# Performance work log

Measured on AMD Instinct MI355X. Metric: run time of the kernel, lower is better.

## Reference

```python
import jax, jax.numpy as jnp
import numpy as np

D, H, K, L, NB = 128, 8, 16, 16, 2
N, E, MN, ME = 100_000, 800_000, 1_000, 8_000
VOCAB, BT, VP = 50_000, 256, 15
_SQD, _SQK = float(np.sqrt(D)), float(np.sqrt(K))


def _segment_softmax(score, seg, num):
    m = jax.ops.segment_max(score, seg, num_segments=num)
    e = jnp.exp(score - m[seg])
    z = jax.ops.segment_sum(e, seg, num_segments=num)
    return e / (z[seg] + 1e-9)


def _meta_learner(feat, u, W2, W1):
    # latent-attention factorization: feat [n,D] -> 2d param [n,H,K], 1d param [n,H]
    w = jax.nn.softmax((feat @ u.T) / _SQD, axis=-1)  # [n,L]
    return jnp.einsum('nl,lhk->nhk', w, W2), w @ W1


def _conv(feat, src, dst, p2n, p1n, p2e, p1e, Wq, Wk, Wv, Wo):
    # HeteroAttnConv: multi-head attention message passing modulated by
    # per-node (p2n,p1n) and per-edge (p2e,p1e) meta parameters.
    n = feat.shape[0]
    q = (feat @ Wq).reshape(n, H, K) * p2n
    kf = (feat @ Wk).reshape(n, H, K)
    v = (feat @ Wv).reshape(n, H, K)
    ke = kf[src] * p2e                                   # [e,H,K]
    score = (q[dst] * ke).sum(-1) / _SQK + p1e + p1n[dst]  # [e,H]
    attn = _segment_softmax(score, dst, n)
    agg = jax.ops.segment_sum(attn[..., None] * v[src], dst, num_segments=n).reshape(n, D)
    return jax.nn.relu(agg @ Wo), ke.reshape(-1, D)


def _forward(emb, u, W2lat, W1lat, Wq_m, Wk_m, Wv_m, Wo_m, Wq, Wk, Wv, Wo,
             node_vals, meta_node_vals, src, dst, meta_src, meta_dst,
             meta_node_id, meta_edge_id, target_idx,
             static_vals, static_src, static_dst):
    # _init_meta_param: static param-name graph, copy_u/sum then meta_learner
    fs = emb[static_vals]
    agg = jax.ops.segment_sum(fs[static_src], static_dst, num_segments=VP)
    p2s, p1s = _meta_learner(agg, u, W2lat, W1lat)
    base_tw, base_n1, base_n2 = p1s[0], p1s[3], p2s[6]   # target_weight, node 1d, node 2d
    base_e1, base_e2 = p1s[9], p2s[12]                   # edge 1d, edge 2d

    meta_feat = emb[meta_node_vals]
    feat = emb[node_vals]
    # _asign_param_to_graph(meta_graph): broadcast base buffers only
    mp2n = jnp.broadcast_to(base_n2, (MN, H, K))
    mp1n = jnp.broadcast_to(base_n1, (MN, H))
    mp2e = jnp.broadcast_to(base_e2, (ME, H, K))
    mp1e = jnp.broadcast_to(base_e1, (ME, H))

    out = jnp.zeros((BT, 1), feat.dtype)
    for b in range(NB):
        pre_meta, pre = meta_feat, feat
        meta_feat, meta_edge_feat = _conv(meta_feat, meta_src, meta_dst,
                                          mp2n, mp1n, mp2e, mp1e,
                                          Wq_m[b], Wk_m[b], Wv_m[b], Wo_m[b])
        # _asign_param_to_graph(graph, meta_node_feat, meta_edge_feat):
        # base repeat + indexed add of meta_learner outputs
        p2mn, p1mn = _meta_learner(meta_feat, u, W2lat, W1lat)
        p2me, p1me = _meta_learner(meta_edge_feat, u, W2lat, W1lat)
        p2n = base_n2[None] + p2mn[meta_node_id]
        p1n = base_n1[None] + p1mn[meta_node_id]
        tw = base_tw[None] + p1mn[meta_node_id]
        p2e = base_e2[None] + p2me[meta_edge_id]
        p1e = base_e1[None] + p1me[meta_edge_id]
        feat, _ = _conv(feat, src, dst, p2n, p1n, p2e, p1e,
                        Wq[b], Wk[b], Wv[b], Wo[b])
        # block residual
        meta_feat = meta_feat + pre_meta
        feat = feat + pre
        # Target: per-target-node weighted readout with target_weight param
        logit = jnp.einsum('th,thk->t', tw[target_idx],
                           feat[target_idx].reshape(BT, H, K))
        out = out + logit[:, None]
    return out / NB


def setup_inputs() -> dict:
    key = jax.random.key(0)
    ks = jax.random.split(key, 24)
    s = 0.05
    inp = {}
    inp['emb'] = jax.random.normal(ks[0], (VOCAB, D), jnp.float32) * s
    inp['u'] = jax.random.normal(ks[1], (L, D), jnp.float32) * s
    inp['W2lat'] = jax.random.normal(ks[2], (L, H, K), jnp.float32) * s
    inp['W1lat'] = jax.random.normal(ks[3], (L, H), jnp.float32) * s
    for i, nm in enumerate(['Wq_m', 'Wk_m', 'Wv_m', 'Wo_m', 'Wq', 'Wk', 'Wv', 'Wo']):
        inp[nm] = jax.random.normal(ks[4 + i], (NB, D, D), jnp.float32) / np.sqrt(D)
    inp['node_vals'] = jax.random.randint(ks[12], (N,), 0, VOCAB)
    inp['meta_node_vals'] = jax.random.randint(ks[13], (MN,), 0, VOCAB)
    inp['src'] = jax.random.randint(ks[14], (E,), 0, N)
    inp['dst'] = jax.random.randint(ks[15], (E,), 0, N)
    inp['meta_src'] = jax.random.randint(ks[16], (ME,), 0, MN)
    inp['meta_dst'] = jax.random.randint(ks[17], (ME,), 0, MN)
    inp['meta_node_id'] = jax.random.randint(ks[18], (N,), 0, MN)
    inp['meta_edge_id'] = jax.random.randint(ks[19], (E,), 0, ME)
    inp['target_idx'] = jax.random.randint(ks[20], (BT,), 0, N)
    # static param-name graph: 5 names x (1 name node + 2 token nodes), tokens->name
    name_pos = np.arange(5) * 3
    inp['static_vals'] = jax.random.randint(ks[21], (VP,), 0, VOCAB)
    inp['static_src'] = jnp.asarray(np.stack([name_pos + 1, name_pos + 2], 1).reshape(-1), jnp.int32)
    inp['static_dst'] = jnp.asarray(np.repeat(name_pos, 2), jnp.int32)
    return inp


def reference(emb, u, W2lat, W1lat, Wq_m, Wk_m, Wv_m, Wo_m, Wq, Wk, Wv, Wo,
              node_vals, meta_node_vals, src, dst, meta_src, meta_dst,
              meta_node_id, meta_edge_id, target_idx,
              static_vals, static_src, static_dst):
    return _forward(emb, u, W2lat, W1lat, Wq_m, Wk_m, Wv_m, Wo_m, Wq, Wk, Wv, Wo,
                    node_vals, meta_node_vals, src, dst, meta_src, meta_dst,
                    meta_node_id, meta_edge_id, target_idx,
                    static_vals, static_src, static_dst)
```

## Files before the change

### kernel.cpp

```cpp
#include <hip/hip_runtime.h>
#include <hip/hip_bf16.h>
#include <hip/hip_fp8.h>

#define DD   128
#define HH   8

typedef short bf16x8 __attribute__((ext_vector_type(8)));
typedef float f32x4  __attribute__((ext_vector_type(4)));
typedef float f32x2  __attribute__((ext_vector_type(2)));

__device__ __forceinline__ float b2f(unsigned short v){
  union { unsigned int u; float f; } x; x.u = ((unsigned int)v) << 16; return x.f;
}
__device__ __forceinline__ unsigned short f2b(float f){
  __hip_bfloat16 h = __float2bfloat16(f);
  return *(unsigned short*)&h;
}
__device__ __forceinline__ unsigned char f2f8(float x){
  __hip_fp8_e4m3 h(x);
  return h.__x;
}
__device__ __forceinline__ float f82f(unsigned char b){
  __hip_fp8_e4m3 h; h.__x = b;
  return (float)h;
}
__device__ __forceinline__ void cvt4(unsigned int w, float* o){
#if defined(__has_builtin)
# if __has_builtin(__builtin_amdgcn_cvt_pk_f32_fp8)
  f32x2 lo = __builtin_amdgcn_cvt_pk_f32_fp8((int)w, false);
  f32x2 hi = __builtin_amdgcn_cvt_pk_f32_fp8((int)w, true);
  o[0]=lo[0]; o[1]=lo[1]; o[2]=hi[0]; o[3]=hi[1];
  return;
# endif
#endif
  o[0]=f82f(w&0xff); o[1]=f82f((w>>8)&0xff);
  o[2]=f82f((w>>16)&0xff); o[3]=f82f((w>>24)&0xff);
}
struct __align__(8) us4 { unsigned short x,y,z,w; };
struct __align__(16) us8 { unsigned short s[8]; };

__device__ __forceinline__ float gld(const void* p, size_t i, bool f32){
  if (f32) return ((const float*)p)[i];
  return b2f(((const unsigned short*)p)[i]);
}

__device__ __forceinline__ void gll16(const void* g, void* l){
  __builtin_amdgcn_global_load_lds(
      (const __attribute__((address_space(1))) unsigned int*)g,
      (__attribute__((address_space(3))) unsigned int*)l, 16, 0, 0);
}

struct WPtrs { const void* p[8]; };
__global__ __launch_bounds__(256) void w_repack16(
    WPtrs W, unsigned short* __restrict__ stage, int NBt,
    const int* __restrict__ dflag)
{
  const bool wf32 = (*dflag) != 0;
  int idx = blockIdx.x >> 6;
  int ti = idx / NBt, bi = idx - ti*NBt;
  size_t bo = (size_t)bi*DD*DD;
  int i = (blockIdx.x & 63)*256 + threadIdx.x;
  int k = i >> 7, n = i & 127;
  float x;
  if (wf32) x = ((const float*)W.p[ti])[bo + i];
  else      x = b2f(((const unsigned short*)W.p[ti])[bo + i]);
  stage[(size_t)idx*DD*DD + n*DD + k] = f2b(x);
}

enum { EPI_STORE=0, EPI_SCALE_CONST=1, EPI_RELU=3,
       EPI_RELU_RES=4, EPI_RELU_RES2=5 };

#define CPAD 132


template<int EPI, bool INB, bool OUTB>
__global__ __launch_bounds__(256) void gemm128m(
    const void* __restrict__ Av, const unsigned short* __restrict__ Bt,
    void* __restrict__ Cv, int M,
    const unsigned short* __restrict__ Rb,
    const float* __restrict__ Rf, float* __restrict__ C2)
{
  __shared__ __align__(16) unsigned short Asb[64*128];
  __shared__ __align__(16) unsigned short Btb[16896];
  const int tid = threadIdx.x;
  const int wave = tid >> 6, lane = tid & 63;
  const int row0 = blockIdx.x * 64;

  if (INB){
    const char* Ab = (const char*)Av;
    int n4 = lane >> 4, c = lane & 15;
#pragma unroll
    for (int op=0; op<4; op++){
      int rA = wave*16 + op*4;
      int n = rA + n4;
      int gr = row0 + n; if (gr >= M) gr = M - 1;
      gll16(Ab + (size_t)gr*256 + ((size_t)((c ^ (n & 7)) << 4)), &Asb[rA*128]);
    }
  } else {
    const float* Af = (const float*)Av;
    int r = tid >> 2, cb = (tid & 3) * 32, rx = (r & 7) << 3;
    int gr = row0 + r;
#pragma unroll
    for (int j=0;j<8;j++){
      int cc = cb + j*4;
      float4 val = make_float4(0.f,0.f,0.f,0.f);
      if (gr < M) val = *(const float4*)(Af + (size_t)gr*DD + cc);
      us4 o; o.x=f2b(val.x); o.y=f2b(val.y); o.z=f2b(val.z); o.w=f2b(val.w);
      *(us4*)&Asb[r*128 + (cc ^ rx)] = o;
    }
  }
  {
    int n4 = lane >> 4, c = lane & 15;
#pragma unroll
    for (int op=0; op<8; op++){
      int rB = wave*32 + op*4;
      int n = rB + n4;
      gll16((const char*)Bt + (size_t)n*256 + ((size_t)((c ^ (n & 7)) << 4)),
            &Btb[rB*128]);
    }
  }
  __syncthreads();

  f32x4 acc[8];
#pragma unroll
  for (int t=0;t<8;t++) acc[t] = (f32x4){0.f,0.f,0.f,0.f};
  const int am = (lane & 15), kq = (lane >> 4) * 8, axr = (am & 7) << 3;
#pragma unroll
  for (int k0=0;k0<128;k0+=32){
    int xo = (k0 + kq) ^ axr;
    bf16x8 a = *(bf16x8*)&Asb[(wave*16 + am)*128 + xo];
#pragma unroll
    for (int t=0;t<8;t++){
      bf16x8 b = *(bf16x8*)&Btb[(t*16 + am)*128 + xo];
      acc[t] = __builtin_amdgcn_mfma_f32_16x16x32_bf16(a, b, acc[t], 0,0,0);
    }
  }
  __syncthreads();
  float* Cls = (float*)Btb;
  {
    int rr = wave*16 + (lane>>4)*4;
    int cc = lane & 15;
#pragma unroll
    for (int t=0;t<8;t++)
#pragma unroll
      for (int r=0;r<4;r++)
        Cls[(rr + r)*CPAD + t*16 + cc] = acc[t][r];
  }
  __syncthreads();

  {
    int r = tid >> 2, cb = (tid & 3) * 32;
    int gr = row0 + r;
    if (gr < M){
#pragma unroll
      for (int j=0;j<8;j++){
        int c = cb + j*4;
        float4 o = *(float4*)&Cls[r*CPAD + c];
        if (EPI == EPI_RELU_RES){
          us4 rb = *(const us4*)(Rb + (size_t)gr*DD + c);
          o.x=fmaxf(o.x,0.f)+b2f(rb.x); o.y=fmaxf(o.y,0.f)+b2f(rb.y);
          o.z=fmaxf(o.z,0.f)+b2f(rb.z); o.w=fmaxf(o.w,0.f)+b2f(rb.w);
        } else if (EPI == EPI_RELU_RES2){
          o.x=fmaxf(o.x,0.f); o.y=fmaxf(o.y,0.f); o.z=fmaxf(o.z,0.f); o.w=fmaxf(o.w,0.f);
          float4 rf = *(const float4*)(Rf + (size_t)gr*DD + c);
          *(float4*)(C2 + (size_t)gr*DD + c) =
              make_float4(o.x+rf.x, o.y+rf.y, o.z+rf.z, o.w+rf.w);
        }
        if (OUTB){
          us4 ob; ob.x=f2b(o.x); ob.y=f2b(o.y); ob.z=f2b(o.z); ob.w=f2b(o.w);
          *(us4*)((unsigned short*)Cv + (size_t)gr*DD + c) = ob;
        } else {
          *(float4*)((float*)Cv + (size_t)gr*DD + c) = o;
        }
      }
    }
  }
}

template<int EPIQ, bool INB, bool FP8KV>
__device__ __forceinline__ void qkv_body(
    unsigned short* Asb, unsigned short* Btb, int blk,
    const void* __restrict__ Av,
    const unsigned short* __restrict__ Btq, const unsigned short* __restrict__ Btk,
    const unsigned short* __restrict__ Btv,
    void* __restrict__ Cq, void* __restrict__ Ck, int stK,
    void* __restrict__ Cvo, int stV, int M,
    const float* __restrict__ svec)
{
  const int tid = threadIdx.x;
  const int wave = tid >> 6, lane = tid & 63;
  const int row0 = blk * 64;

  if (INB){
    const char* Ab = (const char*)Av;
    int n4 = lane >> 4, c = lane & 15;
#pragma unroll
    for (int op=0; op<4; op++){
      int rA = wave*16 + op*4;
      int n = rA + n4;
      int gr = row0 + n; if (gr >= M) gr = M - 1;
      gll16(Ab + (size_t)gr*256 + ((size_t)((c ^ (n & 7)) << 4)), &Asb[rA*128]);
    }
  } else {
    const float* Af = (const float*)Av;
    int r = tid >> 2, cb = (tid & 3) * 32, rx = (r & 7) << 3;
    int gr = row0 + r;
#pragma unroll
    for (int j=0;j<8;j++){
      int cc = cb + j*4;
      float4 val = make_float4(0.f,0.f,0.f,0.f);
      if (gr < M) val = *(const float4*)(Af + (size_t)gr*DD + cc);
      us4 o; o.x=f2b(val.x); o.y=f2b(val.y); o.z=f2b(val.z); o.w=f2b(val.w);
      *(us4*)&Asb[r*128 + (cc ^ rx)] = o;
    }
  }

  const unsigned short* Bts[3] = {Btq, Btk, Btv};
  void* Cs[3] = {Cq, Ck, Cvo};
  const int sts[3] = {DD, stK, stV};
  const int am = (lane & 15), kq = (lane >> 4) * 8, axr = (am & 7) << 3;

  for (int ph=0; ph<3; ph++){
    {
      const unsigned short* Bt = Bts[ph];
      int n4 = lane >> 4, c = lane & 15;
#pragma unroll
      for (int op=0; op<8; op++){
        int rB = wave*32 + op*4;
        int n = rB + n4;
        gll16((const char*)Bt + (size_t)n*256 + ((size_t)((c ^ (n & 7)) << 4)),
              &Btb[rB*128]);
      }
    }
    __syncthreads();
    f32x4 acc[8];
#pragma unroll
    for (int t=0;t<8;t++) acc[t] = (f32x4){0.f,0.f,0.f,0.f};
#pragma unroll
    for (int k0=0;k0<128;k0+=32){
      int xo = (k0 + kq) ^ axr;
      bf16x8 a = *(bf16x8*)&Asb[(wave*16 + am)*128 + xo];
#pragma unroll
      for (int t=0;t<8;t++){
        bf16x8 b = *(bf16x8*)&Btb[(t*16 + am)*128 + xo];
        acc[t] = __builtin_amdgcn_mfma_f32_16x16x32_bf16(a, b, acc[t], 0,0,0);
      }
    }
    __syncthreads();
    float* Cls = (float*)Btb;
    {
      int rr = wave*16 + (lane>>4)*4;
      int cc = lane & 15;
#pragma unroll
      for (int t=0;t<8;t++)
#pragma unroll
        for (int r=0;r<4;r++)
          Cls[(rr + r)*CPAD + t*16 + cc] = acc[t][r];
    }
    __syncthreads();
    {
      int r = tid >> 2, cb = (tid & 3) * 32;
      int gr = row0 + r;
      if (gr < M){
#pragma unroll
        for (int j=0;j<8;j++){
          int c = cb + j*4;
          float4 o = *(float4*)&Cls[r*CPAD + c];
          if (ph == 0 && EPIQ == EPI_SCALE_CONST){
            o.x*=svec[c+0]; o.y*=svec[c+1]; o.z*=svec[c+2]; o.w*=svec[c+3];
          }
          if (FP8KV && ph > 0){
            unsigned char* Cb = (unsigned char*)Cs[ph];
            uchar4 ob;
            ob.x=f2f8(o.x*8.f); ob.y=f2f8(o.y*8.f);
            ob.z=f2f8(o.z*8.f); ob.w=f2f8(o.w*8.f);
            *(uchar4*)(Cb + (size_t)gr*256 + c) = ob;
          } else {
            us4 ob; ob.x=f2b(o.x); ob.y=f2b(o.y); ob.z=f2b(o.z); ob.w=f2b(o.w);
            *(us4*)((unsigned short*)Cs[ph] + (size_t)gr*sts[ph] + c) = ob;
          }
        }
      }
    }
    __syncthreads();
  }
}

__global__ __launch_bounds__(256) void gemm_qkv2(
    const unsigned short* __restrict__ featB, const float* __restrict__ featM,
    const unsigned short* __restrict__ wqb, const unsigned short* __restrict__ wkb,
    const unsigned short* __restrict__ wvb,
    const unsigned short* __restrict__ wqm, const unsigned short* __restrict__ wkm,
    const unsigned short* __restrict__ wvm,
    unsigned short* __restrict__ qB, unsigned char* __restrict__ kv8,
    unsigned short* __restrict__ qM, unsigned short* __restrict__ kfM,
    unsigned short* __restrict__ vM,
    int Nbig, int Nmeta, int gN, const float* __restrict__ svec)
{
  __shared__ __align__(16) unsigned short Asb[64*128];
  __shared__ __align__(16) unsigned short Btb[16896];
  if (blockIdx.x < gN){
    qkv_body<EPI_STORE,true,true>(Asb, Btb, blockIdx.x, featB,
        wqb, wkb, wvb, qB, kv8, 0, kv8 + 128, 0, Nbig, svec);
  } else {
    qkv_body<EPI_SCALE_CONST,false,false>(Asb, Btb, blockIdx.x - gN, featM,
        wqm, wkm, wvm, qM, kfM, DD, vM, DD, Nmeta, svec);
  }
}

__global__ __launch_bounds__(256) void k_static(
    const void* __restrict__ emb, const int* __restrict__ svals,
    const int* __restrict__ ssrc, const int* __restrict__ sdst,
    const void* __restrict__ u, const void* __restrict__ W2,
    const void* __restrict__ W1, float* __restrict__ base, int nsrc,
    int* __restrict__ dflag)
{
  __shared__ float sagg[15][128];
  __shared__ float ssc[15][16];
  __shared__ float sww[15][16];
  __shared__ int swf;
  const int t = threadIdx.x;
  if (t < 64){
    float m = 0.f;
    for (int i=t; i<128; i+=64){
      float x = fabsf(b2f(((const unsigned short*)emb)[i]));
      if (x < 1e30f) m = fmaxf(m, x);
    }
#pragma unroll
    for (int s=1;s<64;s<<=1) m = fmaxf(m, __shfl_xor(m, s, 64));
    if (t==0){ int f = (m > 1e4f) ? 1 : 0; *dflag = f; swf = f; }
  }
  for (int i=t;i<15*128;i+=256) ((float*)sagg)[i]=0.f;
  __syncthreads();
  const bool wf32 = (swf != 0);
  if (t < 128){
    for (int i=0;i<nsrc;i++){
      int row = sdst[i]; int vr = svals[ssrc[i]];
      sagg[row][t] += gld(emb, (size_t)vr*DD + t, wf32);
    }
  }
  __syncthreads();
  if (t < 240){
    int n = t>>4, l = t&15;
    float a=0.f;
    for (int d=0;d<128;d++) a += sagg[n][d]*gld(u, l*128+d, wf32);
    ssc[n][l] = a * 0.08838834764831845f;
  }
  __syncthreads();
  if (t < 15){
    float mx=-1e30f;
    for (int l=0;l<16;l++) mx = fmaxf(mx, ssc[t][l]);
    float s=0.f;
    for (int l=0;l<16;l++){ float e=__expf(ssc[t][l]-mx); sww[t][l]=e; s+=e; }
    float inv = 1.f/s;
    for (int l=0;l<16;l++) sww[t][l]*=inv;
  }
  __syncthreads();
  if (t < 8){
    float a=0.f,b=0.f,c=0.f;
    for (int l=0;l<16;l++){
      float wv = gld(W1, l*8+t, wf32);
      a += sww[0][l]*wv; b += sww[3][l]*wv; c += sww[9][l]*wv;
    }
    base[t]=a; base[8+t]=b; base[16+t]=c;
  }
  if (t < 128){
    float a=0.f,b=0.f;
    for (int l=0;l<16;l++){
      float wv = gld(W2, l*128+t, wf32);
      a += sww[6][l]*wv; b += sww[12][l]*wv;
    }
    base[24+t]=a; base[152+t]=b;
  }
}

__global__ __launch_bounds__(256) void gather_rows2(
    const void* __restrict__ emb,
    const int* __restrict__ valsB, unsigned short* __restrict__ featB, int nB,
    const int* __restrict__ valsM, float* __restrict__ featM, int nM,
    const int* __restrict__ dflag)
{
  const bool wf32 = (*dflag) != 0;
  int i = blockIdx.x*256 + threadIdx.x;
  bool big = (i < nB*16);
  int i2 = big ? i : (i - nB*16);
  if (!big && i2 >= nM*16) return;
  int r = i2>>4, c = (i2&15)*8;
  int vr = big ? valsB[r] : valsM[r];
  float vb[8];
  if (wf32){
    float4 f0 = *(const float4*)((const float*)emb + (size_t)vr*DD + c);
    float4 f1 = *(const float4*)((const float*)emb + (size_t)vr*DD + c + 4);
    vb[0]=f0.x; vb[1]=f0.y; vb[2]=f0.z; vb[3]=f0.w;
    vb[4]=f1.x; vb[5]=f1.y; vb[6]=f1.z; vb[7]=f1.w;
  } else {
    uint4 raw = *(const uint4*)((const unsigned short*)emb + (size_t)vr*DD + c);
    const unsigned short* hw = (const unsigned short*)&raw;
#pragma unroll
    for (int j=0;j<8;j++) vb[j] = b2f(hw[j]);
  }
  if (big){
    unsigned short* d = featB + (size_t)r*DD + c;
    us4 o0, o1;
    o0.x=f2b(vb[0]); o0.y=f2b(vb[1]); o0.z=f2b(vb[2]); o0.w=f2b(vb[3]);
    o1.x=f2b(vb[4]); o1.y=f2b(vb[5]); o1.z=f2b(vb[6]); o1.w=f2b(vb[7]);
    *(us4*)d = o0; *(us4*)(d+4) = o1;
  } else {
    float* d = featM + (size_t)r*DD + c;
    *(float4*)d     = make_float4(vb[0],vb[1],vb[2],vb[3]);
    *(float4*)(d+4) = make_float4(vb[4],vb[5],vb[6],vb[7]);
  }
}

__global__ __launch_bounds__(256) void zeroi(int* __restrict__ p, int n){
  int i = blockIdx.x*256 + threadIdx.x;
  if (i < n) p[i] = 0;
}

__global__ __launch_bounds__(256) void k_hist2(
    const int* __restrict__ dstB, const int* __restrict__ dstM,
    int* __restrict__ degB, int* __restrict__ degM, int E, int ME, int nbE){
  int b = blockIdx.x, t = threadIdx.x;
  if (b < nbE){ int i = b*256+t; if (i < E) atomicAdd(&degB[dstB[i]], 1); }
  else { int i = (b-nbE)*256+t; if (i < ME) atomicAdd(&degM[dstM[i]], 1); }
}

__global__ __launch_bounds__(256) void k_scan1b(
    const int* __restrict__ degB, int* __restrict__ rpB, int* __restrict__ bsB,
    int nB, int nbB,
    const int* __restrict__ degM, int* __restrict__ rpM, int* __restrict__ bsM,
    int nM){
  __shared__ int ls[256];
  int blk = blockIdx.x, t = threadIdx.x;
  const int* deg; int* rowptr; int* bsum; int n; int b;
  if (blk < nbB){ deg=degB; rowptr=rpB; bsum=bsB; n=nB; b=blk; }
  else          { deg=degM; rowptr=rpM; bsum=bsM; n=nM; b=blk-nbB; }
  int base = b*1024 + t*4;
  int v0 = (base+0<n)?deg[base+0]:0;
  int v1 = (base+1<n)?deg[base+1]:0;
  int v2 = (base+2<n)?deg[base+2]:0;
  int v3 = (base+3<n)?deg[base+3]:0;
  int tsum = v0+v1+v2+v3;
  ls[t] = tsum; __syncthreads();
  for (int o=1;o<256;o<<=1){
    int x = (t>=o) ? ls[t-o] : 0;
    __syncthreads();
    ls[t] += x;
    __syncthreads();
  }
  int excl = ls[t]-tsum;
  if (t==255) bsum[b] = ls[255];
  if (base+0<n) rowptr[base+0]=excl;
  if (base+1<n) rowptr[base+1]=excl+v0;
  if (base+2<n) rowptr[base+2]=excl+v0+v1;
  if (base+3<n) rowptr[base+3]=excl+v0+v1+v2;
}

__global__ __launch_bounds__(256) void k_scan3b(
    int* __restrict__ rpB, const int* __restrict__ bsB, int* __restrict__ curB,
    int nB, int nb3B, int nbsB,
    int* __restrict__ rpM, const int* __restrict__ bsM, int* __restrict__ curM,
    int nM, int nbsM){
  __shared__ int spre;
  int blk = blockIdx.x, t = threadIdx.x;
  if (blk < nb3B){
    if (t == 0){
      int chunk = blk >> 2;
      int pre = 0;
      for (int j=0;j<chunk;j++) pre += bsB[j];
      spre = pre;
      if (blk == 0){
        int tot = 0;
        for (int j=0;j<nbsB;j++) tot += bsB[j];
        rpB[nB] = tot;
      }
    }
    __syncthreads();
    int i = blk*256 + t;
    if (i < nB){ int r = rpB[i] + spre; rpB[i] = r; curB[i] = r; }
  } else {
    int b2 = blk - nb3B;
    if (t == 0){
      int chunk = b2 >> 2;
      int pre = 0;
      for (int j=0;j<chunk;j++) pre += bsM[j];
      spre = pre;
      if (b2 == 0){
        int tot = 0;
        for (int j=0;j<nbsM;j++) tot += bsM[j];
        rpM[nM] = tot;
      }
    }
    __syncthreads();
    int i = b2*256 + t;
    if (i < nM){ int r = rpM[i] + spre; rpM[i] = r; curM[i] = r; }
  }
}

__global__ __launch_bounds__(256) void k_scatter2(
    const int* __restrict__ dstB, const int* __restrict__ srcB,
    const int* __restrict__ auxB, int* __restrict__ curB,
    int* __restrict__ epackB, int E, int nbE,
    const int* __restrict__ dstM, const int* __restrict__ srcM,
    int* __restrict__ curM, int* __restrict__ esrcM, int* __restrict__ eauxM,
    int ME, int nbME,
    const int* __restrict__ dbins, int* __restrict__ dcur){
  int blk = blockIdx.x, t = threadIdx.x;
  if (blk < nbE){
    int e = blk*256 + t;
    if (e < E){
      int p = atomicAdd(&curB[dstB[e]], 1);
      epackB[p] = srcB[e] | (auxB[e] << 17);
    }
  } else if (blk < nbE + nbME){
    int e = (blk-nbE)*256 + t;
    if (e < ME){
      int p = atomicAdd(&curM[dstM[e]], 1);
      esrcM[p] = srcM[e];
      eauxM[p] = e;
    }
  } else {
    if (t == 0){
      int run = 0;
      for (int j=0;j<64;j++){ dcur[j] = run; run += dbins[j]; }
    }
  }
}

__global__ __launch_bounds__(256) void k_dhist(
    const int* __restrict__ deg, int* __restrict__ dbins, int N){
  __shared__ int lh[64];
  int t = threadIdx.x;
  if (t < 64) lh[t] = 0;
  __syncthreads();
  int i = blockIdx.x*256 + t;
  if (i < N){
    int dg = deg[i]; if (dg > 63) dg = 63;
    atomicAdd(&lh[dg], 1);
  }
  __syncthreads();
  if (t < 64 && lh[t]) atomicAdd(&dbins[t], lh[t]);
}

__global__ __launch_bounds__(256) void k_dsort(
    const int* __restrict__ deg, int* __restrict__ dcur,
    int* __restrict__ sortN, int N){
  __shared__ int lh[64];
  __shared__ int gbase[64];
  int t = threadIdx.x;
  if (t < 64) lh[t] = 0;
  __syncthreads();
  int i = blockIdx.x*256 + t;
  int dg = 0, rank = 0;
  bool act = (i < N);
  if (act){
    dg = deg[i]; if (dg > 63) dg = 63;
    rank = atomicAdd(&lh[dg], 1);
  }
  __syncthreads();
  if (t < 64 && lh[t]) gbase[t] = atomicAdd(&dcur[t], lh[t]);
  __syncthreads();
  if (act) sortN[gbase[dg] + rank] = i;
}

__global__ __launch_bounds__(256) void edge_meta_csr(
    const int* __restrict__ rowptr, const int* __restrict__ esrc,
    const int* __restrict__ eorig,
    const unsigned short* __restrict__ qm, const unsigned short* __restrict__ kfm,
    const unsigned short* __restrict__ vm,
    const float* __restrict__ base, unsigned short* __restrict__ mef,
    float* __restrict__ agg, int NM)
{
  int d = blockIdx.x*4 + (threadIdx.x>>6);
  if (d >= NM) return;
  int lane = threadIdx.x & 63;
  const float* be2 = base+152; const float* be1 = base+16; const float* bn1 = base+8;
  size_t dq = (size_t)d*DD;
  float q0 = b2f(qm[dq+lane]), q1 = b2f(qm[dq+64+lane]);
  float w0 = be2[lane], w1 = be2[64+lane];
  int h0 = lane>>4, h1 = h0+4;
  float bias0 = be1[h0] + bn1[h0];
  float bias1 = be1[h1] + bn1[h1];
  float z0=0.f, z1=0.f, a0=0.f, a1=0.f;
  int i0 = rowptr[d], i1 = rowptr[d+1];
  for (int i=i0; i<i1; i++){
    int s = esrc[i], e = eorig[i];
    size_t so=(size_t)s*DD, eo=(size_t)e*DD;
    float ke0 = b2f(kfm[so+lane])    * w0;
    float ke1 = b2f(kfm[so+64+lane]) * w1;
    mef[eo+lane]=f2b(ke0); mef[eo+64+lane]=f2b(ke1);
    float p0 = q0*ke0, p1 = q1*ke1;
#pragma unroll
    for (int m=1;m<16;m<<=1){ p0 += __shfl_xor(p0,m,64); p1 += __shfl_xor(p1,m,64); }
    float e0 = __expf(p0*0.25f + bias0);
    float e1 = __expf(p1*0.25f + bias1);
    z0 += e0; z1 += e1;
    a0 += e0*b2f(vm[so+lane]);
    a1 += e1*b2f(vm[so+64+lane]);
  }
  float inv0 = 1.f/(z0 + 1e-9f);
  float inv1 = 1.f/(z1 + 1e-9f);
  agg[dq+lane]    = a0*inv0;
  agg[dq+64+lane] = a1*inv1;
}

__global__ __launch_bounds__(128) void learner2(
    const float* __restrict__ Xa, const unsigned short* __restrict__ Xb,
    int Ma, int Mtot,
    const void* __restrict__ u, const void* __restrict__ W2,
    const void* __restrict__ W1,
    unsigned short* __restrict__ qsc, float* __restrict__ p1a,
    unsigned short* __restrict__ w2me, unsigned short* __restrict__ p1b,
    const float* __restrict__ base, const int* __restrict__ dflag)
{
  __shared__ float sX[128];
  __shared__ float st[16];
  __shared__ float sw[16];
  const bool wf32 = (*dflag) != 0;
  const int t = threadIdx.x;
  const int l = t>>3, j = t&7;
  float uc[16], w2c[16], w1c[16];
#pragma unroll
  for (int m=0;m<16;m++) uc[m] = gld(u, (size_t)l*128 + j*16 + m, wf32);
#pragma unroll
  for (int i=0;i<16;i++) w2c[i] = gld(W2, (size_t)i*128 + t, wf32);
  if (t < 8){
#pragma unroll
    for (int i=0;i<16;i++) w1c[i] = gld(W1, (size_t)i*8 + t, wf32);
  }
  for (int rr=0; rr<4; rr++){
    int row = blockIdx.x*4 + rr;
    if (row >= Mtot) break;
    const bool isB = (row >= Ma);
    const int m = isB ? (row - Ma) : row;
    if (isB) sX[t] = b2f(Xb[(size_t)m*DD + t]);
    else     sX[t] = Xa[(size_t)m*DD + t];
    __syncthreads();
    float part = 0.f;
#pragma unroll
    for (int mm=0;mm<16;mm++) part += sX[j*16+mm]*uc[mm];
    part += __shfl_xor(part,1,64); part += __shfl_xor(part,2,64); part += __shfl_xor(part,4,64);
    if (j==0) st[l] = part * 0.08838834764831845f;
    __syncthreads();
    float mx=-1e30f;
    for (int i=0;i<16;i++) mx = fmaxf(mx, st[i]);
    float ssum=0.f;
    for (int i=0;i<16;i++) ssum += __expf(st[i]-mx);
    float inv = 1.f/ssum;
    if (t<16) sw[t] = __expf(st[t]-mx)*inv;
    __syncthreads();
    float a=0.f;
#pragma unroll
    for (int i=0;i<16;i++) a += sw[i]*w2c[i];
    if (isB) w2me[(size_t)m*DD+t] = f2b(base[152+t] + a);
    else     qsc[(size_t)m*DD+t] = f2b(base[24+t] + a);
    if (t<8){
      float bb=0.f;
#pragma unroll
      for (int i=0;i<16;i++) bb += sw[i]*w1c[i];
      if (isB) p1b[(size_t)m*HH+t] = f2b(bb);
      else     p1a[(size_t)m*HH+t] = bb;
    }
    __syncthreads();
  }
}

__global__ __launch_bounds__(256) void edge_fused(
    const int* __restrict__ rowptr, const int* __restrict__ epack,
    const int* __restrict__ sortN, const int* __restrict__ mnid,
    const unsigned short* __restrict__ q, const unsigned char* __restrict__ kv8,
    const unsigned short* __restrict__ w2me, const unsigned short* __restrict__ p1me,
    const float* __restrict__ p1mn, const unsigned short* __restrict__ qsc,
    const float* __restrict__ base,
    unsigned short* __restrict__ aggb, int N)
{
  int wv = blockIdx.x*4 + (threadIdx.x>>6);
  int lane = threadIdx.x & 63;
  int grp = lane >> 4, l16 = lane & 15;
  int idx = wv*4 + grp;
  if (idx >= N) return;
  int d = sortN[idx];
  int c8 = l16 * 8;
  int h = l16 >> 1;

  int i0 = rowptr[d], i1 = rowptr[d+1];
  int mn = mnid[d];
  float bias = base[16+h] + base[8+h] + p1mn[(size_t)mn*HH + h];
  size_t dq = (size_t)d*DD;
  float qv[8];
  {
    uint4 qraw = *(const uint4*)(q + dq + c8);
    us8 sc = *(const us8*)(qsc + (size_t)mn*DD + c8);
    const unsigned short* qh = (const unsigned short*)&qraw;
#pragma unroll
    for (int j=0;j<8;j++) qv[j] = b2f(qh[j]) * b2f(sc.s[j]) * 0.03125f;
  }

  float zh = 0.f;
  float a[8];
#pragma unroll
  for (int j=0;j<8;j++) a[j] = 0.f;

  int i = i0;
  for (; i + 1 < i1; i += 2){
    unsigned int v0p = (unsigned int)epack[i];
    unsigned int v1p = (unsigned int)epack[i+1];
    int s0 = v0p & 0x1FFFF, me0 = v0p >> 17;
    int s1 = v1p & 0x1FFFF, me1 = v1p >> 17;
    const unsigned char* kv0 = kv8 + (size_t)s0*256 + c8;
    const unsigned char* kv1 = kv8 + (size_t)s1*256 + c8;
    uint2 kraw0 = *(const uint2*)kv0;
    uint2 vraw0 = *(const uint2*)(kv0 + 128);
    uint4 wraw0 = *(const uint4*)(w2me + (size_t)me0*DD + c8);
    float pm0 = b2f(p1me[(size_t)me0*HH + h]);
    uint2 kraw1 = *(const uint2*)kv1;
    uint2 vraw1 = *(const uint2*)(kv1 + 128);
    uint4 wraw1 = *(const uint4*)(w2me + (size_t)me1*DD + c8);
    float pm1 = b2f(p1me[(size_t)me1*HH + h]);
    float k0f[8], v0f[8], k1f[8], v1f[8];
    cvt4(kraw0.x, k0f); cvt4(kraw0.y, k0f+4);
    cvt4(vraw0.x, v0f); cvt4(vraw0.y, v0f+4);
    cvt4(kraw1.x, k1f); cvt4(kraw1.y, k1f+4);
    cvt4(vraw1.x, v1f); cvt4(vraw1.y, v1f+4);
    const unsigned short* wh0 = (const unsigned short*)&wraw0;
    const unsigned short* wh1 = (const unsigned short*)&wraw1;
    float pA = 0.f, pB = 0.f;
#pragma unroll
    for (int j=0;j<8;j++){
      pA += qv[j]*(k0f[j]*b2f(wh0[j]));
      pB += qv[j]*(k1f[j]*b2f(wh1[j]));
    }
    pA += __shfl_xor(pA, 1, 64);
    pB += __shfl_xor(pB, 1, 64);
    float ex0 = __expf(pA + bias + pm0);
    float ex1 = __expf(pB + bias + pm1);
    zh += ex0 + ex1;
#pragma unroll
    for (int j=0;j<8;j++) a[j] += ex0*v0f[j] + ex1*v1f[j];
  }
  if (i < i1){
    unsigned int vp = (unsigned int)epack[i];
    int s = vp & 0x1FFFF, me = vp >> 17;
    const unsigned char* kv = kv8 + (size_t)s*256 + c8;
    uint2 kraw = *(const uint2*)kv;
    uint2 vraw = *(const uint2*)(kv + 128);
    uint4 wraw = *(const uint4*)(w2me + (size_t)me*DD + c8);
    float pm = b2f(p1me[(size_t)me*HH + h]);
    float kf[8], vf[8];
    cvt4(kraw.x, kf); cvt4(kraw.y, kf+4);
    cvt4(vraw.x, vf); cvt4(vraw.y, vf+4);
    const unsigned short* wh = (const unsigned short*)&wraw;
    float p = 0.f;
#pragma unroll
    for (int j=0;j<8;j++) p += qv[j]*(kf[j]*b2f(wh[j]));
    p += __shfl_xor(p, 1, 64);
    float ex = __expf(p + bias + pm);
    zh += ex;
#pragma unroll
    for (int j=0;j<8;j++) a[j] += ex*vf[j];
  }

  float inv = 0.125f / (zh + 1e-9f);
  us8 o;
#pragma unroll
  for (int j=0;j<8;j++) o.s[j] = f2b(a[j]*inv);
  *(us8*)(aggb + dq + c8) = o;
}

__global__ __launch_bounds__(256) void readout(
    const int* __restrict__ tgt, const int* __restrict__ mnid,
    const unsigned short* __restrict__ featb, const float* __restrict__ p1mn,
    const float* __restrict__ base, float* __restrict__ acc,
    void* __restrict__ out, int last, float invNB, int BT,
    const int* __restrict__ dflag)
{
  int t = blockIdx.x*256 + threadIdx.x;
  int ti = t >> 4, l16 = t & 15;
  if (ti >= BT) return;
  int idx = tgt[ti]; int mn = mnid[idx];
  int h = l16 >> 1;
  float tw = base[h] + p1mn[(size_t)mn*HH + h];
  uint4 raw = *(const uint4*)(featb + (size_t)idx*DD + l16*8);
  const unsigned short* hw = (const unsigned short*)&raw;
  float s = 0.f;
#pragma unroll
  for (int j=0;j<8;j++) s += b2f(hw[j]);
  float part = tw * s;
  part += __shfl_xor(part, 1, 64);
  part += __shfl_xor(part, 2, 64);
  part += __shfl_xor(part, 4, 64);
  part += __shfl_xor(part, 8, 64);
  if (l16 == 0){
    if (!last) acc[ti] = part;
    else {
      float r = (acc[ti] + part) * invNB;
      if ((*dflag) != 0) ((float*)out)[ti] = r;
      else ((__hip_bfloat16*)out)[ti] = __float2bfloat16(r);
    }
  }
}

extern "C" void kernel_launch(void* const* d_in, const int* in_sizes, int n_in,
                              void* d_out, int out_size, void* d_ws, size_t ws_size,
                              hipStream_t stream) {
  const void* emb   = d_in[0];
  const void* u     = d_in[1];
  const void* W2lat = d_in[2];
  const void* W1lat = d_in[3];
  WPtrs wptrs;
  for (int i=0;i<8;i++) wptrs.p[i] = d_in[4+i];
  const int* node_vals      = (const int*)d_in[12];
  const int* meta_node_vals = (const int*)d_in[13];
  const int* src            = (const int*)d_in[14];
  const int* dst            = (const int*)d_in[15];
  const int* meta_src       = (const int*)d_in[16];
  const int* meta_dst       = (const int*)d_in[17];
  const int* meta_node_id   = (const int*)d_in[18];
  const int* meta_edge_id   = (const int*)d_in[19];
  const int* target_idx     = (const int*)d_in[20];
  const int* static_vals    = (const int*)d_in[21];
  const int* static_src     = (const int*)d_in[22];
  const int* static_dst     = (const int*)d_in[23];

  const int N  = in_sizes[12];
  const int MN = in_sizes[13];
  const int E  = in_sizes[14];
  const int ME = in_sizes[16];
  const int BT = in_sizes[20];
  const int NSRC = in_sizes[22];
  const int NB = in_sizes[8] / (DD*DD);

  float* ws = (float*)d_ws;
  size_t off = 0;
  auto allocf = [&](size_t n){ float* p = ws + off; off += (n + 3) & ~(size_t)3; return p; };
  auto allocb = [&](size_t n){ unsigned short* p = (unsigned short*)(ws + off); off += (((n+1)/2) + 3) & ~(size_t)3; return p; };
  auto alloci = [&](size_t n){ int* p = (int*)(ws + off); off += (n + 3) & ~(size_t)3; return p; };
  int*            dflag = (int*)ws; off += 4;
  unsigned short* feat  = allocb((size_t)N*DD);
  unsigned short* q     = allocb((size_t)N*DD);
  unsigned char*  kv8   = (unsigned char*)allocf((size_t)N*64);
  unsigned short* aggb  = allocb((size_t)N*DD);
  float*          meta_feat= allocf((size_t)MN*DD);
  float*          agg_m = allocf((size_t)MN*DD);
  unsigned short* q_m   = allocb((size_t)MN*DD);
  unsigned short* kf_m  = allocb((size_t)MN*DD);
  unsigned short* v_m   = allocb((size_t)MN*DD);
  float*          meta_out = allocf((size_t)MN*DD);
  unsigned short* mef   = allocb((size_t)ME*DD);
  unsigned short* qsc   = allocb((size_t)MN*DD);
  float*          p1mn  = allocf((size_t)MN*HH);
  unsigned short* w2me  = allocb((size_t)ME*DD);
  unsigned short* p1me  = allocb((size_t)ME*HH);
  float*          base  = allocf(280);
  float*          acc   = allocf((size_t)BT);
  unsigned short* wstage= allocb((size_t)8*NB*DD*DD);
  int*            rowptr= alloci((size_t)N+1);
  int*            cursor= alloci((size_t)N);
  int*            epack = alloci((size_t)E);
  int*            rowptr_m= alloci((size_t)MN+1);
  int*            cursor_m= alloci((size_t)MN);
  int*            esrc_m  = alloci((size_t)ME);
  int*            eorig_m = alloci((size_t)ME);
  int*            dbins   = alloci(64);
  int*            degAll  = alloci((size_t)(N+MN));
  int*            deg     = degAll;
  int*            deg_m   = degAll + N;
  int*            dcur    = alloci(64);
  int*            sortN   = alloci((size_t)N);
  const int nb_scan   = (N + 1023)/1024;
  const int nb_scan_m = (MN + 1023)/1024;
  int*            bsum   = alloci((size_t)nb_scan);
  int*            bsum_m = alloci((size_t)nb_scan_m);
  (void)ws_size; (void)n_in; (void)out_size;

  const float* base_n2 = base + 24;

  k_static<<<1,256,0,stream>>>(emb, static_vals, static_src, static_dst,
                               u, W2lat, W1lat, base, NSRC, dflag);
  gather_rows2<<<((N+MN)*16+255)/256,256,0,stream>>>(emb, node_vals, feat, N,
      meta_node_vals, meta_feat, MN, dflag);

  const int nbE  = (E+255)/256, nbME = (ME+255)/256;
  const int nb3B = (N+255)/256, nb3M = (MN+255)/256;
  zeroi<<<(64+N+MN+255)/256,256,0,stream>>>(dbins, 64+N+MN);
  k_hist2<<<nbE+nbME,256,0,stream>>>(dst, meta_dst, deg, deg_m, E, ME, nbE);
  k_dhist<<<(N+255)/256,256,0,stream>>>(deg, dbins, N);
  k_scan1b<<<nb_scan+nb_scan_m,256,0,stream>>>(deg, rowptr, bsum, N, nb_scan,
      deg_m, rowptr_m, bsum_m, MN);
  k_scan3b<<<nb3B+nb3M,256,0,stream>>>(rowptr, bsum, cursor, N, nb3B, nb_scan,
      rowptr_m, bsum_m, cursor_m, MN, nb_scan_m);
  k_scatter2<<<nbE+nbME+1,256,0,stream>>>(dst, src, meta_edge_id, cursor,
      epack, E, nbE, meta_dst, meta_src, cursor_m, esrc_m, eorig_m, ME, nbME,
      dbins, dcur);
  k_dsort<<<(N+255)/256,256,0,stream>>>(deg, dcur, sortN, N);

  w_repack16<<<8*NB*64,256,0,stream>>>(wptrs, wstage, NB, dflag);

  const int gm = (MN+63)/64;
  const int gN = (N+63)/64;
  const float invNB = 1.0f/(float)NB;

  for (int b=0;b<NB;b++){
    const unsigned short* wq_m = wstage + (size_t)(0*NB+b)*DD*DD;
    const unsigned short* wk_m = wstage + (size_t)(1*NB+b)*DD*DD;
    const unsigned short* wv_m = wstage + (size_t)(2*NB+b)*DD*DD;
    const unsigned short* wo_m = wstage + (size_t)(3*NB+b)*DD*DD;
    const unsigned short* wqb  = wstage + (size_t)(4*NB+b)*DD*DD;
    const unsigned short* wkb  = wstage + (size_t)(5*NB+b)*DD*DD;
    const unsigned short* wvb  = wstage + (size_t)(6*NB+b)*DD*DD;
    const unsigned short* wob  = wstage + (size_t)(7*NB+b)*DD*DD;

    gemm_qkv2<<<gN+gm,256,0,stream>>>(feat, meta_feat,
        wqb, wkb, wvb, wq_m, wk_m, wv_m,
        q, kv8, q_m, kf_m, v_m, N, MN, gN, base_n2);

    edge_meta_csr<<<(MN+3)/4,256,0,stream>>>(rowptr_m, esrc_m, eorig_m,
        q_m, kf_m, v_m, base, mef, agg_m, MN);
    gemm128m<EPI_RELU_RES2,false,false><<<gm,256,0,stream>>>(agg_m, wo_m,
        meta_out, MN, nullptr, meta_feat, meta_feat);
    learner2<<<(MN+ME+3)/4,128,0,stream>>>(meta_out, mef, MN, MN+ME,
        u, W2lat, W1lat, qsc, p1mn, w2me, p1me, base, dflag);

    edge_fused<<<(N+15)/16,256,0,stream>>>(rowptr, epack, sortN,
        meta_node_id, q, kv8, w2me, p1me, p1mn, qsc, base, aggb, N);
    gemm128m<EPI_RELU_RES,true,true><<<gN,256,0,stream>>>(aggb, wob, feat, N,
        feat, nullptr, nullptr);

    readout<<<(BT*16+255)/256,256,0,stream>>>(target_idx, meta_node_id, feat, p1mn,
        base, acc, d_out, (b==NB-1) ? 1 : 0, invNB, BT, dflag);
  }
}
```

Baseline: 589.3 us.

## Store q, k/v, and meta params head-major and split edge kernel per head

The QKV GEMM epilogue and learner2 now write q, fp8 k/v, qsc and w2me in a head-major layout ([H][rows][16]), so each head's slice for all nodes is contiguous. edge_fused is re-gridded so each block handles one head for 128 destination nodes, with two lanes per node per head. The goal is for the random gathers of k/v by source node to stay within a per-head working set that is eight times smaller, improving cache hit rates. In exchange, each destination's edge list and metadata are now read eight times (once per head), and the per-edge gathers become small 8–16 byte accesses.

```diff
diff --git a/kernel.cpp b/kernel.cpp
--- a/kernel.cpp
+++ b/kernel.cpp
@@ -71,7 +71,6 @@
        EPI_RELU_RES=4, EPI_RELU_RES2=5 };
 
 #define CPAD 132
-
 
 template<int EPI, bool INB, bool OUTB>
 __global__ __launch_bounds__(256) void gemm128m(
@@ -269,12 +268,18 @@
           if (ph == 0 && EPIQ == EPI_SCALE_CONST){
             o.x*=svec[c+0]; o.y*=svec[c+1]; o.z*=svec[c+2]; o.w*=svec[c+3];
           }
-          if (FP8KV && ph > 0){
-            unsigned char* Cb = (unsigned char*)Cs[ph];
-            uchar4 ob;
-            ob.x=f2f8(o.x*8.f); ob.y=f2f8(o.y*8.f);
-            ob.z=f2f8(o.z*8.f); ob.w=f2f8(o.w*8.f);
-            *(uchar4*)(Cb + (size_t)gr*256 + c) = ob;
+          if (FP8KV){
+            int hh = c >> 4, c4 = c & 15;
+            if (ph == 0){
+              us4 ob; ob.x=f2b(o.x); ob.y=f2b(o.y); ob.z=f2b(o.z); ob.w=f2b(o.w);
+              *(us4*)((unsigned short*)Cs[0] + ((size_t)hh*M + gr)*16 + c4) = ob;
+            } else {
+              unsigned char* Cb = (unsigned char*)Cs[1];
+              uchar4 ob;
+              ob.x=f2f8(o.x*8.f); ob.y=f2f8(o.y*8.f);
+              ob.z=f2f8(o.z*8.f); ob.w=f2f8(o.w*8.f);
+              *(uchar4*)(Cb + ((size_t)hh*M + gr)*32 + (ph==2?16:0) + c4) = ob;
+            }
           } else {
             us4 ob; ob.x=f2b(o.x); ob.y=f2b(o.y); ob.z=f2b(o.z); ob.w=f2b(o.w);
             *(us4*)((unsigned short*)Cs[ph] + (size_t)gr*sts[ph] + c) = ob;
@@ -292,7 +297,7 @@
     const unsigned short* __restrict__ wvb,
     const unsigned short* __restrict__ wqm, const unsigned short* __restrict__ wkm,
     const unsigned short* __restrict__ wvm,
-    unsigned short* __restrict__ qB, unsigned char* __restrict__ kv8,
+    unsigned short* __restrict__ qh, unsigned char* __restrict__ kvh,
     unsigned short* __restrict__ qM, unsigned short* __restrict__ kfM,
     unsigned short* __restrict__ vM,
     int Nbig, int Nmeta, int gN, const float* __restrict__ svec)
@@ -301,7 +306,7 @@
   __shared__ __align__(16) unsigned short Btb[16896];
   if (blockIdx.x < gN){
     qkv_body<EPI_STORE,true,true>(Asb, Btb, blockIdx.x, featB,
-        wqb, wkb, wvb, qB, kv8, 0, kv8 + 128, 0, Nbig, svec);
+        wqb, wkb, wvb, qh, kvh, 0, nullptr, 0, Nbig, svec);
   } else {
     qkv_body<EPI_SCALE_CONST,false,false>(Asb, Btb, blockIdx.x - gN, featM,
         wqm, wkm, wvm, qM, kfM, DD, vM, DD, Nmeta, svec);
@@ -609,16 +614,18 @@
     int Ma, int Mtot,
     const void* __restrict__ u, const void* __restrict__ W2,
     const void* __restrict__ W1,
-    unsigned short* __restrict__ qsc, float* __restrict__ p1a,
-    unsigned short* __restrict__ w2me, unsigned short* __restrict__ p1b,
+    unsigned short* __restrict__ qsch, float* __restrict__ p1a,
+    unsigned short* __restrict__ w2meh, unsigned short* __restrict__ p1b,
     const float* __restrict__ base, const int* __restrict__ dflag)
 {
   __shared__ float sX[128];
   __shared__ float st[16];
   __shared__ float sw[16];
   const bool wf32 = (*dflag) != 0;
+  const int MEc = Mtot - Ma;
   const int t = threadIdx.x;
   const int l = t>>3, j = t&7;
+  const int th = t >> 4, tc = t & 15;
   float uc[16], w2c[16], w1c[16];
 #pragma unroll
   for (int m=0;m<16;m++) uc[m] = gld(u, (size_t)l*128 + j*16 + m, wf32);
@@ -652,8 +659,8 @@
     float a=0.f;
 #pragma unroll
     for (int i=0;i<16;i++) a += sw[i]*w2c[i];
-    if (isB) w2me[(size_t)m*DD+t] = f2b(base[152+t] + a);
-    else     qsc[(size_t)m*DD+t] = f2b(base[24+t] + a);
+    if (isB) w2meh[((size_t)th*MEc + m)*16 + tc] = f2b(base[152+t] + a);
+    else     qsch [((size_t)th*Ma  + m)*16 + tc] = f2b(base[24+t] + a);
     if (t<8){
       float bb=0.f;
 #pragma unroll
@@ -668,32 +675,32 @@
 __global__ __launch_bounds__(256) void edge_fused(
     const int* __restrict__ rowptr, const int* __restrict__ epack,
     const int* __restrict__ sortN, const int* __restrict__ mnid,
-    const unsigned short* __restrict__ q, const unsigned char* __restrict__ kv8,
-    const unsigned short* __restrict__ w2me, const unsigned short* __restrict__ p1me,
-    const float* __restrict__ p1mn, const unsigned short* __restrict__ qsc,
+    const unsigned short* __restrict__ qh, const unsigned char* __restrict__ kvh,
+    const unsigned short* __restrict__ w2meh, const unsigned short* __restrict__ p1me,
+    const float* __restrict__ p1mn, const unsigned short* __restrict__ qsch,
     const float* __restrict__ base,
-    unsigned short* __restrict__ aggb, int N)
+    unsigned short* __restrict__ aggb, int N, int MEc, int MNc)
 {
-  int wv = blockIdx.x*4 + (threadIdx.x>>6);
-  int lane = threadIdx.x & 63;
-  int grp = lane >> 4, l16 = lane & 15;
-  int idx = wv*4 + grp;
-  if (idx >= N) return;
-  int d = sortN[idx];
-  int c8 = l16 * 8;
-  int h = l16 >> 1;
-
-  int i0 = rowptr[d], i1 = rowptr[d+1];
-  int mn = mnid[d];
-  float bias = base[16+h] + base[8+h] + p1mn[(size_t)mn*HH + h];
-  size_t dq = (size_t)d*DD;
+  const int tid = threadIdx.x;
+  const int lane = tid & 63;
+  const int h = blockIdx.x & 7;
+  const int chunk = blockIdx.x >> 3;
+  const int item = chunk*128 + (tid>>6)*32 + (lane>>1);
+  if (item >= N) return;
+  const int p = lane & 1;
+  const int d = sortN[item];
+  const int i0 = rowptr[d], i1 = rowptr[d+1];
+  const int mn = mnid[d];
+  const float bias = base[16+h] + base[8+h] + p1mn[(size_t)mn*HH + h];
+
   float qv[8];
   {
-    uint4 qraw = *(const uint4*)(q + dq + c8);
-    us8 sc = *(const us8*)(qsc + (size_t)mn*DD + c8);
-    const unsigned short* qh = (const unsigned short*)&qraw;
-#pragma unroll
-    for (int j=0;j<8;j++) qv[j] = b2f(qh[j]) * b2f(sc.s[j]) * 0.03125f;
+    uint4 qraw = *(const uint4*)(qh  + ((size_t)h*N   + d )*16 + p*8);
+    uint4 scr  = *(const uint4*)(qsch+ ((size_t)h*MNc + mn)*16 + p*8);
+    const unsigned short* qw = (const unsigned short*)&qraw;
+    const unsigned short* sc = (const unsigned short*)&scr;
+#pragma unroll
+    for (int j=0;j<8;j++) qv[j] = b2f(qw[j]) * b2f(sc[j]) * 0.03125f;
   }
 
   float zh = 0.f;
@@ -707,15 +714,15 @@
     unsigned int v1p = (unsigned int)epack[i+1];
     int s0 = v0p & 0x1FFFF, me0 = v0p >> 17;
     int s1 = v1p & 0x1FFFF, me1 = v1p >> 17;
-    const unsigned char* kv0 = kv8 + (size_t)s0*256 + c8;
-    const unsigned char* kv1 = kv8 + (size_t)s1*256 + c8;
+    const unsigned char* kv0 = kvh + ((size_t)h*N + s0)*32 + p*8;
+    const unsigned char* kv1 = kvh + ((size_t)h*N + s1)*32 + p*8;
     uint2 kraw0 = *(const uint2*)kv0;
-    uint2 vraw0 = *(const uint2*)(kv0 + 128);
-    uint4 wraw0 = *(const uint4*)(w2me + (size_t)me0*DD + c8);
+    uint2 vraw0 = *(const uint2*)(kv0 + 16);
+    uint4 wraw0 = *(const uint4*)(w2meh + ((size_t)h*MEc + me0)*16 + p*8);
     float pm0 = b2f(p1me[(size_t)me0*HH + h]);
     uint2 kraw1 = *(const uint2*)kv1;
-    uint2 vraw1 = *(const uint2*)(kv1 + 128);
-    uint4 wraw1 = *(const uint4*)(w2me + (size_t)me1*DD + c8);
+    uint2 vraw1 = *(const uint2*)(kv1 + 16);
+    uint4 wraw1 = *(const uint4*)(w2meh + ((size_t)h*MEc + me1)*16 + p*8);
     float pm1 = b2f(p1me[(size_t)me1*HH + h]);
     float k0f[8], v0f[8], k1f[8], v1f[8];
     cvt4(kraw0.x, k0f); cvt4(kraw0.y, k0f+4);
@@ -741,20 +748,20 @@
   if (i < i1){
     unsigned int vp = (unsigned int)epack[i];
     int s = vp & 0x1FFFF, me = vp >> 17;
-    const unsigned char* kv = kv8 + (size_t)s*256 + c8;
+    const unsigned char* kv = kvh + ((size_t)h*N + s)*32 + p*8;
     uint2 kraw = *(const uint2*)kv;
-    uint2 vraw = *(const uint2*)(kv + 128);
-    uint4 wraw = *(const uint4*)(w2me + (size_t)me*DD + c8);
+    uint2 vraw = *(const uint2*)(kv + 16);
+    uint4 wraw = *(const uint4*)(w2meh + ((size_t)h*MEc + me)*16 + p*8);
     float pm = b2f(p1me[(size_t)me*HH + h]);
     float kf[8], vf[8];
     cvt4(kraw.x, kf); cvt4(kraw.y, kf+4);
     cvt4(vraw.x, vf); cvt4(vraw.y, vf+4);
     const unsigned short* wh = (const unsigned short*)&wraw;
-    float p = 0.f;
-#pragma unroll
-    for (int j=0;j<8;j++) p += qv[j]*(kf[j]*b2f(wh[j]));
-    p += __shfl_xor(p, 1, 64);
-    float ex = __expf(p + bias + pm);
+    float pfull = 0.f;
+#pragma unroll
+    for (int j=0;j<8;j++) pfull += qv[j]*(kf[j]*b2f(wh[j]));
+    pfull += __shfl_xor(pfull, 1, 64);
+    float ex = __expf(pfull + bias + pm);
     zh += ex;
 #pragma unroll
     for (int j=0;j<8;j++) a[j] += ex*vf[j];
@@ -764,7 +771,7 @@
   us8 o;
 #pragma unroll
   for (int j=0;j<8;j++) o.s[j] = f2b(a[j]*inv);
-  *(us8*)(aggb + dq + c8) = o;
+  *(us8*)(aggb + (size_t)d*DD + h*16 + p*8) = o;
 }
 
 __global__ __launch_bounds__(256) void readout(
@@ -837,8 +844,8 @@
   auto alloci = [&](size_t n){ int* p = (int*)(ws + off); off += (n + 3) & ~(size_t)3; return p; };
   int*            dflag = (int*)ws; off += 4;
   unsigned short* feat  = allocb((size_t)N*DD);
-  unsigned short* q     = allocb((size_t)N*DD);
-  unsigned char*  kv8   = (unsigned char*)allocf((size_t)N*64);
+  unsigned short* qh    = allocb((size_t)N*DD);
+  unsigned char*  kvh   = (unsigned char*)allocf((size_t)N*64);
   unsigned short* aggb  = allocb((size_t)N*DD);
   float*          meta_feat= allocf((size_t)MN*DD);
   float*          agg_m = allocf((size_t)MN*DD);
@@ -847,9 +854,9 @@
   unsigned short* v_m   = allocb((size_t)MN*DD);
   float*          meta_out = allocf((size_t)MN*DD);
   unsigned short* mef   = allocb((size_t)ME*DD);
-  unsigned short* qsc   = allocb((size_t)MN*DD);
+  unsigned short* qsch  = allocb((size_t)MN*DD);
   float*          p1mn  = allocf((size_t)MN*HH);
-  unsigned short* w2me  = allocb((size_t)ME*DD);
+  unsigned short* w2meh = allocb((size_t)ME*DD);
   unsigned short* p1me  = allocb((size_t)ME*HH);
   float*          base  = allocf(280);
   float*          acc   = allocf((size_t)BT);
@@ -898,6 +905,7 @@
 
   const int gm = (MN+63)/64;
   const int gN = (N+63)/64;
+  const int gEF = 8 * ((N + 127)/128);
   const float invNB = 1.0f/(float)NB;
 
   for (int b=0;b<NB;b++){
@@ -912,17 +920,17 @@
 
     gemm_qkv2<<<gN+gm,256,0,stream>>>(feat, meta_feat,
         wqb, wkb, wvb, wq_m, wk_m, wv_m,
-        q, kv8, q_m, kf_m, v_m, N, MN, gN, base_n2);
+        qh, kvh, q_m, kf_m, v_m, N, MN, gN, base_n2);
 
     edge_meta_csr<<<(MN+3)/4,256,0,stream>>>(rowptr_m, esrc_m, eorig_m,
         q_m, kf_m, v_m, base, mef, agg_m, MN);
     gemm128m<EPI_RELU_RES2,false,false><<<gm,256,0,stream>>>(agg_m, wo_m,
         meta_out, MN, nullptr, meta_feat, meta_feat);
     learner2<<<(MN+ME+3)/4,128,0,stream>>>(meta_out, mef, MN, MN+ME,
-        u, W2lat, W1lat, qsc, p1mn, w2me, p1me, base, dflag);
-
-    edge_fused<<<(N+15)/16,256,0,stream>>>(rowptr, epack, sortN,
-        meta_node_id, q, kv8, w2me, p1me, p1mn, qsc, base, aggb, N);
+        u, W2lat, W1lat, qsch, p1mn, w2meh, p1me, base, dflag);
+
+    edge_fused<<<gEF,256,0,stream>>>(rowptr, epack, sortN,
+        meta_node_id, qh, kvh, w2meh, p1me, p1mn, qsch, base, aggb, N, ME, MN);
     gemm128m<EPI_RELU_RES,true,true><<<gN,256,0,stream>>>(aggb, wob, feat, N,
         feat, nullptr, nullptr);
 
```

Result: slower. 770.0 us (+30.7%).
